# Kernel tuning notes

Measured on AMD Instinct MI355X. Metric: run time of the kernel, lower is better.

## Reference

```python
import jax, jax.numpy as jnp
import numpy as np


def setup_inputs() -> dict:
    key = jax.random.key(0)
    k1, k2, k3, k4 = jax.random.split(key, 4)
    T, B, D_in, D_out = 512, 128, 512, 512
    X = jax.random.normal(k1, (T, B, D_in), dtype=jnp.float32)
    # torch nn.Linear default init: U(-1/sqrt(fan_in), 1/sqrt(fan_in))
    lim_in = 1.0 / np.sqrt(D_in)
    lim_h = 1.0 / np.sqrt(D_out)
    W_in = jax.random.uniform(k2, (D_out, D_in), jnp.float32, -lim_in, lim_in)
    W_h = jax.random.uniform(k3, (D_out, D_out), jnp.float32, -lim_h, lim_h)
    b_h = jax.random.uniform(k4, (D_out,), jnp.float32, -lim_h, lim_h)
    return {"X": X, "W_in": W_in, "W_h": W_h, "b_h": b_h}


def reference(X, W_in, W_h, b_h):
    # X: [T, B, D_in]. h_{t+1} = sigmoid(x_t @ W_in^T + h_t @ W_h^T + b_h)
    B = X.shape[1]
    D_out = W_h.shape[0]
    # Precompute all input projections in one big GEMM (same math).
    Xproj = jnp.einsum('tbi,oi->tbo', X, W_in)  # [T, B, D_out]
    h0 = jnp.zeros((B, D_out), dtype=X.dtype)

    def step(h, xp):
        h_new = jax.nn.sigmoid(xp + h @ W_h.T + b_h)
        return h_new, None

    h_last, _ = jax.lax.scan(step, h0, Xproj)
    return h_last
```

## Files before the change

### kernel.cpp

```cpp
#include <hip/hip_runtime.h>
#include <hip/hip_bf16.h>
#include <stdint.h>

typedef _Float16 f16;
typedef _Float16 f16x2 __attribute__((ext_vector_type(2)));
typedef _Float16 f16x4 __attribute__((ext_vector_type(4)));
typedef _Float16 f16x8 __attribute__((ext_vector_type(8)));
typedef float f32x4 __attribute__((ext_vector_type(4)));
typedef int   i32x4 __attribute__((ext_vector_type(4)));

#define T_STEPS 512
#define BATCH   128
#define DD      512
#define LOG2E   1.44269504088896f

#define XP_OFF  0
#define WF_OFF  (67108864)
#define WHQ_OFF (67108864 + 524288)
#define SC_OFF  (67108864 + 524288 + 262144)

__device__ __forceinline__ f16x2 pk(float a, float b) {
    return __builtin_bit_cast(f16x2, __builtin_amdgcn_cvt_pkrtz(a, b));
}

__device__ __forceinline__ float fast_exp2(float x) {
#if __has_builtin(__builtin_amdgcn_exp2f)
    return __builtin_amdgcn_exp2f(x);
#else
    return exp2f(x);
#endif
}

__device__ __forceinline__ float fast_rcp(float x) {
#if __has_builtin(__builtin_amdgcn_rcpf)
    return __builtin_amdgcn_rcpf(x);
#else
    return 1.0f / x;
#endif
}

__device__ __forceinline__ uint32_t pack_u8(float s, int pos, uint32_t old) {
#if __has_builtin(__builtin_amdgcn_cvt_pk_u8_f32)
    return __builtin_amdgcn_cvt_pk_u8_f32(s, pos, old);
#else
    return old | (((uint32_t)(int)s & 0xFF) << (8 * pos));
#endif
}

#define GLDS(g, l) __builtin_amdgcn_global_load_lds(                               \
        (const __attribute__((address_space(1))) void*)(g),                        \
        (__attribute__((address_space(3))) void*)(l), 16, 0, 0)

__global__ __launch_bounds__(256) void prep_kernel(
        const float* __restrict__ Win, f16* __restrict__ Wf) {
    int idx = blockIdx.x * 256 + threadIdx.x;
    if (idx < 262144) Wf[idx] = (f16)Win[idx];
}

__global__ __launch_bounds__(64) void quant_kernel(
        const float* __restrict__ Wh, char* __restrict__ Whq, float* __restrict__ scales) {
    const int o = blockIdx.x, t = threadIdx.x;
    const float* row = Wh + (size_t)o * 512;
    float v[8];
    float m = 0.f;
#pragma unroll
    for (int j = 0; j < 8; j++) { v[j] = row[t * 8 + j]; m = fmaxf(m, fabsf(v[j])); }
#pragma unroll
    for (int off = 32; off > 0; off >>= 1) m = fmaxf(m, __shfl_xor(m, off));
    if (t == 0) scales[o] = -LOG2E * m * (1.0f / (127.0f * 127.0f));
    const float inv = 127.0f / m;
    const int rt = o >> 4, rl = o & 15;
    const int k0 = t * 8;
    const int ks = k0 >> 6, qq = (k0 >> 4) & 3, j0 = k0 & 15;
    const int l = qq * 16 + rl;
    char* dst = Whq + ((size_t)((rt * 8 + ks) * 64 + l)) * 16 + j0;
#pragma unroll
    for (int j = 0; j < 8; j++) dst[j] = (char)rintf(v[j] * inv);
}

__global__ __launch_bounds__(512, 4) void gemm_kernel(
        const float* __restrict__ X, const f16* __restrict__ Wf,
        const float* __restrict__ bias, f16* __restrict__ Xp) {
    const int tid = threadIdx.x;
    const int l = tid & 63, w = tid >> 6;
    const int q = l >> 4, rl = l & 15;
    const int wm = w >> 2, wn = w & 3;
    const int m_blk = blockIdx.y * 128;
    const int n_blk = blockIdx.x * 256;

    __shared__ __align__(16) float As[2][128 * 32];
    __shared__ __align__(16) f16   Bs[2][256 * 32];

    const float* aSrc[2];
#pragma unroll
    for (int c = 0; c < 2; c++)
        aSrc[c] = X + (size_t)(m_blk + w * 16 + c * 8 + (l >> 3)) * 512
                    + (((l & 7) ^ (l >> 3)) << 2);
    const f16* bSrc[2];
#pragma unroll
    for (int c = 0; c < 2; c++)
        bSrc[c] = Wf + (size_t)(n_blk + w * 32 + c * 16 + (l >> 2)) * 512
                     + ((l & 3) << 3);

    f32x4 acc[4][4] = {};
    const int sw0 = (((2 * q)     ^ (rl & 7)) << 2);
    const int sw1 = (((2 * q + 1) ^ (rl & 7)) << 2);

#pragma unroll
    for (int c = 0; c < 2; c++) GLDS(aSrc[c], &As[0][(w * 16 + c * 8) * 32]);
#pragma unroll
    for (int c = 0; c < 2; c++) GLDS(bSrc[c], &Bs[0][(w * 32 + c * 16) * 32]);

    for (int t = 0; t < 16; ++t) {
        const int cur = t & 1;
        __syncthreads();
        if (t < 15) {
            const int kf = (t + 1) * 32;
#pragma unroll
            for (int c = 0; c < 2; c++) GLDS(aSrc[c] + kf, &As[cur ^ 1][(w * 16 + c * 8) * 32]);
#pragma unroll
            for (int c = 0; c < 2; c++) GLDS(bSrc[c] + kf, &Bs[cur ^ 1][(w * 32 + c * 16) * 32]);
        }
        f16x8 af[4], bf[4];
#pragma unroll
        for (int i = 0; i < 4; i++) {
            const int row = wm * 64 + i * 16 + rl;
            const float4 h0 = *(const float4*)&As[cur][row * 32 + sw0];
            const float4 h1 = *(const float4*)&As[cur][row * 32 + sw1];
            f16x2 p0 = pk(h0.x, h0.y), p1 = pk(h0.z, h0.w);
            f16x2 p2 = pk(h1.x, h1.y), p3 = pk(h1.z, h1.w);
            f16x8 tv;
            tv[0] = p0[0]; tv[1] = p0[1]; tv[2] = p1[0]; tv[3] = p1[1];
            tv[4] = p2[0]; tv[5] = p2[1]; tv[6] = p3[0]; tv[7] = p3[1];
            af[i] = tv;
        }
#pragma unroll
        for (int j = 0; j < 4; j++) {
            const int row = wn * 64 + j * 16 + rl;
            bf[j] = *(const f16x8*)&Bs[cur][row * 32 + q * 8];
        }
#pragma unroll
        for (int i = 0; i < 4; i++)
#pragma unroll
            for (int j = 0; j < 4; j++)
                acc[i][j] = __builtin_amdgcn_mfma_f32_16x16x32_f16(af[i], bf[j], acc[i][j], 0, 0, 0);
    }
#pragma unroll
    for (int j = 0; j < 4; j++) {
        const int n = n_blk + wn * 64 + j * 16 + rl;
        const float bn = bias[n];
#pragma unroll
        for (int i = 0; i < 4; i++)
#pragma unroll
            for (int r = 0; r < 4; r++) {
                const int m = m_blk + wm * 64 + i * 16 + q * 4 + r;
                Xp[(size_t)m * 512 + n] = (f16)(-LOG2E * (acc[i][j][r] + bn));
            }
    }
}

__global__ __launch_bounds__(1024) void rnn_kernel(
        const char* __restrict__ Whq, const float* __restrict__ scales,
        const f16* __restrict__ Xp, float* __restrict__ out) {
    const int wg = blockIdx.x;
    const int tid = threadIdx.x;
    const int l = tid & 63, w = tid >> 6;
    const int bl = l & 15;
    const int q = l >> 4;
    const int b = wg * 16 + bl;

    __shared__ __align__(16) uint32_t hT[2][2048];

    i32x4 af[2][8];
    {
        const i32x4* wp = (const i32x4*)Whq;
#pragma unroll
        for (int mt = 0; mt < 2; mt++)
#pragma unroll
            for (int ks = 0; ks < 8; ks++)
                af[mt][ks] = wp[((w * 2 + mt) * 8 + ks) * 64 + l];
    }
    float sc[2][4];
#pragma unroll
    for (int mt = 0; mt < 2; mt++)
#pragma unroll
        for (int r = 0; r < 4; r++)
            sc[mt][r] = scales[w * 32 + mt * 16 + q * 4 + r];

    for (int i = tid; i < 2048; i += 1024) hT[0][i] = 0u;
    __syncthreads();

    const f16* xpb = Xp + (size_t)b * 512 + w * 32 + q * 4;
    f16x4 xn[2];
    xn[0] = *(const f16x4*)(xpb);
    xn[1] = *(const f16x4*)(xpb + 16);

    const float K127 = 1.0f / 127.0f;
    for (int t = 0; t < T_STEPS; t++) {
        f16x4 xc[2];
        xc[0] = xn[0]; xc[1] = xn[1];
        const size_t tn = (size_t)(t < T_STEPS - 1 ? t + 1 : t) * (BATCH * 512);
        xn[0] = *(const f16x4*)(xpb + tn);
        xn[1] = *(const f16x4*)(xpb + tn + 16);

        const int rb = t & 1;
        i32x4 acc[2] = {};
        const uint32_t* hrow = &hT[rb][l * 4];
#pragma unroll
        for (int ks = 0; ks < 8; ks++) {
            i32x4 bfr = *(const i32x4*)(hrow + ks * 256);
            acc[0] = __builtin_amdgcn_mfma_i32_16x16x64_i8(af[0][ks], bfr, acc[0], 0, 0, 0);
            acc[1] = __builtin_amdgcn_mfma_i32_16x16x64_i8(af[1][ks], bfr, acc[1], 0, 0, 0);
        }
#pragma unroll
        for (int mt = 0; mt < 2; mt++) {
            uint32_t pkq = 0;
#pragma unroll
            for (int r = 0; r < 4; r++) {
                float tt = fmaf((float)acc[mt][r], sc[mt][r], (float)xc[mt][r]);
                float e  = fast_exp2(tt);
                float eq = fmaf(e, K127, K127);
                float sg = fast_rcp(eq) + 0.5f;
                pkq = pack_u8(sg, r, pkq);
            }
            hT[1 - rb][(w * 2 + mt) * 64 + bl * 4 + q] = pkq;
        }
        __syncthreads();
    }
#pragma unroll
    for (int mt = 0; mt < 2; mt++) {
        uint32_t pkq = hT[T_STEPS & 1][(w * 2 + mt) * 64 + bl * 4 + q];
        float4 o;
        o.x = (float)((pkq      ) & 0xFF) * K127;
        o.y = (float)((pkq >>  8) & 0xFF) * K127;
        o.z = (float)((pkq >> 16) & 0xFF) * K127;
        o.w = (float)((pkq >> 24) & 0xFF) * K127;
        *(float4*)(out + (size_t)b * 512 + w * 32 + mt * 16 + q * 4) = o;
    }
}

extern "C" void kernel_launch(void* const* d_in, const int* in_sizes, int n_in,
                              void* d_out, int out_size, void* d_ws, size_t ws_size,
                              hipStream_t stream) {
    const float* X   = (const float*)d_in[0];
    const float* Win = (const float*)d_in[1];
    const float* Wh  = (const float*)d_in[2];
    const float* bh  = (const float*)d_in[3];
    float* out = (float*)d_out;
    char* ws = (char*)d_ws;
    f16* Xp      = (f16*)(ws + XP_OFF);
    f16* Wf      = (f16*)(ws + WF_OFF);
    char* Whq    = (char*)(ws + WHQ_OFF);
    float* Sc    = (float*)(ws + SC_OFF);

    prep_kernel<<<1024, 256, 0, stream>>>(Win, Wf);
    quant_kernel<<<512, 64, 0, stream>>>(Wh, Whq, Sc);
    gemm_kernel<<<dim3(2, 512), 512, 0, stream>>>(X, Wf, bh, Xp);
    rnn_kernel<<<8, 1024, 0, stream>>>(Whq, Sc, Xp, out);
}
```

Before: 671.8 us.

## Remap GEMM blocks per XCD, swizzle B LDS, vectorize stores, split RNN MFMA chains

```diff
diff --git a/kernel.cpp b/kernel.cpp
--- a/kernel.cpp
+++ b/kernel.cpp
@@ -85,8 +85,10 @@
     const int l = tid & 63, w = tid >> 6;
     const int q = l >> 4, rl = l & 15;
     const int wm = w >> 2, wn = w & 3;
-    const int m_blk = blockIdx.y * 128;
-    const int n_blk = blockIdx.x * 256;
+    const int blk = blockIdx.x;
+    const int xcd = blk & 7, kk = blk >> 3;
+    const int m_blk = (xcd * 64 + (kk >> 1)) * 128;
+    const int n_blk = (kk & 1) * 256;
 
     __shared__ __align__(16) float As[2][128 * 32];
     __shared__ __align__(16) f16   Bs[2][256 * 32];
@@ -100,11 +102,12 @@
 #pragma unroll
     for (int c = 0; c < 2; c++)
         bSrc[c] = Wf + (size_t)(n_blk + w * 32 + c * 16 + (l >> 2)) * 512
-                     + ((l & 3) << 3);
+                     + (((l & 3) ^ ((l >> 3) & 3)) << 3);
 
     f32x4 acc[4][4] = {};
-    const int sw0 = (((2 * q)     ^ (rl & 7)) << 2);
-    const int sw1 = (((2 * q + 1) ^ (rl & 7)) << 2);
+    const int swA0 = (((2 * q)     ^ (rl & 7)) << 2);
+    const int swA1 = (((2 * q + 1) ^ (rl & 7)) << 2);
+    const int swB  = ((q ^ ((rl >> 1) & 3)) << 3);
 
 #pragma unroll
     for (int c = 0; c < 2; c++) GLDS(aSrc[c], &As[0][(w * 16 + c * 8) * 32]);
@@ -121,41 +124,43 @@
 #pragma unroll
             for (int c = 0; c < 2; c++) GLDS(bSrc[c] + kf, &Bs[cur ^ 1][(w * 32 + c * 16) * 32]);
         }
-        f16x8 af[4], bf[4];
+        f16x8 af4[4], bf4[4];
 #pragma unroll
         for (int i = 0; i < 4; i++) {
             const int row = wm * 64 + i * 16 + rl;
-            const float4 h0 = *(const float4*)&As[cur][row * 32 + sw0];
-            const float4 h1 = *(const float4*)&As[cur][row * 32 + sw1];
+            const float4 h0 = *(const float4*)&As[cur][row * 32 + swA0];
+            const float4 h1 = *(const float4*)&As[cur][row * 32 + swA1];
             f16x2 p0 = pk(h0.x, h0.y), p1 = pk(h0.z, h0.w);
             f16x2 p2 = pk(h1.x, h1.y), p3 = pk(h1.z, h1.w);
             f16x8 tv;
             tv[0] = p0[0]; tv[1] = p0[1]; tv[2] = p1[0]; tv[3] = p1[1];
             tv[4] = p2[0]; tv[5] = p2[1]; tv[6] = p3[0]; tv[7] = p3[1];
-            af[i] = tv;
+            af4[i] = tv;
         }
 #pragma unroll
         for (int j = 0; j < 4; j++) {
             const int row = wn * 64 + j * 16 + rl;
-            bf[j] = *(const f16x8*)&Bs[cur][row * 32 + q * 8];
+            bf4[j] = *(const f16x8*)&Bs[cur][row * 32 + swB];
         }
 #pragma unroll
         for (int i = 0; i < 4; i++)
 #pragma unroll
             for (int j = 0; j < 4; j++)
-                acc[i][j] = __builtin_amdgcn_mfma_f32_16x16x32_f16(af[i], bf[j], acc[i][j], 0, 0, 0);
+                acc[i][j] = __builtin_amdgcn_mfma_f32_16x16x32_f16(bf4[j], af4[i], acc[i][j], 0, 0, 0);
     }
 #pragma unroll
     for (int j = 0; j < 4; j++) {
-        const int n = n_blk + wn * 64 + j * 16 + rl;
-        const float bn = bias[n];
-#pragma unroll
-        for (int i = 0; i < 4; i++)
-#pragma unroll
-            for (int r = 0; r < 4; r++) {
-                const int m = m_blk + wm * 64 + i * 16 + q * 4 + r;
-                Xp[(size_t)m * 512 + n] = (f16)(-LOG2E * (acc[i][j][r] + bn));
-            }
+        const float4 b4 = *(const float4*)&bias[n_blk + wn * 64 + j * 16 + q * 4];
+        const float bb[4] = {b4.x, b4.y, b4.z, b4.w};
+#pragma unroll
+        for (int i = 0; i < 4; i++) {
+            const int m = m_blk + wm * 64 + i * 16 + rl;
+            f16x4 v;
+#pragma unroll
+            for (int r = 0; r < 4; r++)
+                v[r] = (f16)(-LOG2E * (acc[i][j][r] + bb[r]));
+            *(f16x4*)(Xp + (size_t)m * 512 + n_blk + wn * 64 + j * 16 + q * 4) = v;
+        }
     }
 }
 
@@ -191,45 +196,64 @@
     __syncthreads();
 
     const f16* xpb = Xp + (size_t)b * 512 + w * 32 + q * 4;
-    f16x4 xn[2];
-    xn[0] = *(const f16x4*)(xpb);
-    xn[1] = *(const f16x4*)(xpb + 16);
+    f16x4 xn0 = *(const f16x4*)(xpb);
+    f16x4 xn1 = *(const f16x4*)(xpb + 16);
 
     const float K127 = 1.0f / 127.0f;
     for (int t = 0; t < T_STEPS; t++) {
-        f16x4 xc[2];
-        xc[0] = xn[0]; xc[1] = xn[1];
+        f16x4 xc0 = xn0, xc1 = xn1;
         const size_t tn = (size_t)(t < T_STEPS - 1 ? t + 1 : t) * (BATCH * 512);
-        xn[0] = *(const f16x4*)(xpb + tn);
-        xn[1] = *(const f16x4*)(xpb + tn + 16);
+        xn0 = *(const f16x4*)(xpb + tn);
+        xn1 = *(const f16x4*)(xpb + tn + 16);
 
         const int rb = t & 1;
-        i32x4 acc[2] = {};
         const uint32_t* hrow = &hT[rb][l * 4];
+        uint32_t* hwr = &hT[1 - rb][w * 128 + bl * 4 + q];
+
+        i32x4 acc0 = {};
+        __builtin_amdgcn_s_setprio(1);
 #pragma unroll
         for (int ks = 0; ks < 8; ks++) {
             i32x4 bfr = *(const i32x4*)(hrow + ks * 256);
-            acc[0] = __builtin_amdgcn_mfma_i32_16x16x64_i8(af[0][ks], bfr, acc[0], 0, 0, 0);
-            acc[1] = __builtin_amdgcn_mfma_i32_16x16x64_i8(af[1][ks], bfr, acc[1], 0, 0, 0);
-        }
-#pragma unroll
-        for (int mt = 0; mt < 2; mt++) {
-            uint32_t pkq = 0;
-#pragma unroll
-            for (int r = 0; r < 4; r++) {
-                float tt = fmaf((float)acc[mt][r], sc[mt][r], (float)xc[mt][r]);
-                float e  = fast_exp2(tt);
-                float eq = fmaf(e, K127, K127);
-                float sg = fast_rcp(eq) + 0.5f;
-                pkq = pack_u8(sg, r, pkq);
-            }
-            hT[1 - rb][(w * 2 + mt) * 64 + bl * 4 + q] = pkq;
-        }
+            acc0 = __builtin_amdgcn_mfma_i32_16x16x64_i8(af[0][ks], bfr, acc0, 0, 0, 0);
+        }
+        __builtin_amdgcn_s_setprio(0);
+
+        uint32_t pk0 = 0;
+#pragma unroll
+        for (int r = 0; r < 4; r++) {
+            float tt = fmaf((float)acc0[r], sc[0][r], (float)xc0[r]);
+            float e  = fast_exp2(tt);
+            float eq = fmaf(e, K127, K127);
+            float sg = fast_rcp(eq) + 0.5f;
+            pk0 = pack_u8(sg, r, pk0);
+        }
+        hwr[0] = pk0;
+
+        i32x4 acc1 = {};
+        __builtin_amdgcn_s_setprio(1);
+#pragma unroll
+        for (int ks = 0; ks < 8; ks++) {
+            i32x4 bfr = *(const i32x4*)(hrow + ks * 256);
+            acc1 = __builtin_amdgcn_mfma_i32_16x16x64_i8(af[1][ks], bfr, acc1, 0, 0, 0);
+        }
+        __builtin_amdgcn_s_setprio(0);
+
+        uint32_t pk1 = 0;
+#pragma unroll
+        for (int r = 0; r < 4; r++) {
+            float tt = fmaf((float)acc1[r], sc[1][r], (float)xc1[r]);
+            float e  = fast_exp2(tt);
+            float eq = fmaf(e, K127, K127);
+            float sg = fast_rcp(eq) + 0.5f;
+            pk1 = pack_u8(sg, r, pk1);
+        }
+        hwr[64] = pk1;
         __syncthreads();
     }
 #pragma unroll
     for (int mt = 0; mt < 2; mt++) {
-        uint32_t pkq = hT[T_STEPS & 1][(w * 2 + mt) * 64 + bl * 4 + q];
+        uint32_t pkq = hT[T_STEPS & 1][w * 128 + mt * 64 + bl * 4 + q];
         float4 o;
         o.x = (float)((pkq      ) & 0xFF) * K127;
         o.y = (float)((pkq >>  8) & 0xFF) * K127;
@@ -255,6 +279,6 @@
 
     prep_kernel<<<1024, 256, 0, stream>>>(Win, Wf);
     quant_kernel<<<512, 64, 0, stream>>>(Wh, Whq, Sc);
-    gemm_kernel<<<dim3(2, 512), 512, 0, stream>>>(X, Wf, bh, Xp);
+    gemm_kernel<<<1024, 512, 0, stream>>>(X, Wf, bh, Xp);
     rnn_kernel<<<8, 1024, 0, stream>>>(Whq, Sc, Xp, out);
 }
```

Result: slower. 738.1 us (+9.9%).
